# Optimization experiments

Measured on AMD Instinct MI355X. Metric: run time of the kernel, lower is better.

The kernel has to match this reference:

```python
import jax, jax.numpy as jnp
import numpy as np

SCENE = (128, 128, 8)      # (X, Y, Z) voxel grid
VOXEL_SIZE = 0.4
DOWNSAMPLE_Z = 2
NUM_HEADS = 8
NUM_POINTS = 4
LN_EPS = 1e-5


def _pix2vox(depth, K, E, voxel_origin):
    # depth [1,H,W]; K [1,3,3]; E [1,4,4]; voxel_origin [1,3]
    B, H, W = depth.shape
    gx, gy = jnp.meshgrid(jnp.arange(W, dtype=depth.dtype), jnp.arange(H, dtype=depth.dtype))
    pix = jnp.stack([gx, gy])                              # [2,H,W] -> (u, v) after flip in torch
    d = depth[:, None]                                     # [B,1,H,W]
    p_x = jnp.concatenate([pix[None] * d, d], 1).reshape(B, 3, -1)
    p_c = jnp.linalg.inv(K) @ p_x                          # camera coords [B,3,HW]
    p_c = jnp.concatenate([p_c, jnp.ones_like(p_c[:, :1])], 1)
    p_w = jnp.linalg.inv(E) @ p_c                          # world coords [B,4,HW]
    p_v = (jnp.swapaxes(p_w[:, :3], 1, 2) - voxel_origin[:, None, :]) / VOXEL_SIZE - 0.5
    p_v = p_v.at[..., 2].set(p_v[..., 2] / DOWNSAMPLE_Z)
    return jnp.trunc(p_v).astype(jnp.int32)               # torch .long() truncates toward 0


def _voxel_mask(p_v):
    X, Y, Z = SCENE
    p = p_v[0]                                             # [HW,3] (batch asserted == 1)
    valid = ((p[:, 0] >= 0) & (p[:, 0] < X) & (p[:, 1] >= 0) & (p[:, 1] < Y)
             & (p[:, 2] >= 0) & (p[:, 2] < Z))
    flat = jnp.where(valid, (p[:, 0] * Y + p[:, 1]) * Z + p[:, 2], 0)
    return jnp.zeros(X * Y * Z, dtype=bool).at[flat].max(valid)


def _ms_deform_attn(q, feats, ref, Wv, bv, Woff, boff, Wattw, battw, Wout, bout):
    # q [N,C]; feats: list of [C,Hl,Wl]; ref [N,2] normalized (shared across levels)
    N, C = q.shape
    hd = C // NUM_HEADS
    shapes = [(f.shape[1], f.shape[2]) for f in feats]
    L = len(feats)
    flat = jnp.concatenate([f.reshape(C, -1).T for f in feats], 0)      # [Lsum, C]
    value = (flat @ Wv.T + bv).reshape(-1, NUM_HEADS, hd)               # [Lsum, h, hd]
    off = (q @ Woff.T + boff).reshape(N, NUM_HEADS, L, NUM_POINTS, 2)
    w = jax.nn.softmax((q @ Wattw.T + battw).reshape(N, NUM_HEADS, L * NUM_POINTS), -1)
    w = w.reshape(N, NUM_HEADS, L, NUM_POINTS)
    normalizer = jnp.array([[wl, hl] for (hl, wl) in shapes], dtype=q.dtype)  # (W,H) per level
    loc = ref[:, None, None, None, :] + off / normalizer[None, None, :, None, :]
    h_idx = jnp.arange(NUM_HEADS)[None, :, None]
    out = jnp.zeros((N, NUM_HEADS, hd), q.dtype)
    start = 0
    for lvl, (Hl, Wl) in enumerate(shapes):
        v = value[start:start + Hl * Wl]                   # [Hl*Wl, h, hd]
        start += Hl * Wl
        # grid_sample bilinear, align_corners=False, zero padding
        x = loc[:, :, lvl, :, 0] * Wl - 0.5                # [N,h,P]
        y = loc[:, :, lvl, :, 1] * Hl - 0.5
        x0 = jnp.floor(x); y0 = jnp.floor(y)
        lx = x - x0; ly = y - y0
        x0i = x0.astype(jnp.int32); y0i = y0.astype(jnp.int32)
        samp = jnp.zeros((N, NUM_HEADS, NUM_POINTS, hd), q.dtype)
        for dy, dx, wgt in ((0, 0, (1 - lx) * (1 - ly)), (0, 1, lx * (1 - ly)),
                            (1, 0, (1 - lx) * ly), (1, 1, lx * ly)):
            xi = x0i + dx; yi = y0i + dy
            ok = (xi >= 0) & (xi < Wl) & (yi >= 0) & (yi < Hl)
            idx = jnp.where(ok, yi * Wl + xi, 0)
            g = v[idx, h_idx]                              # [N,h,P,hd] per-head gather
            samp = samp + g * (wgt * ok)[..., None]
        out = out + jnp.einsum('nhp,nhpd->nhd', w[:, :, lvl], samp)
    return out.reshape(N, C) @ Wout.T + bout


def _forward(scene_embed, feat0, feat1, feat2, depth, K, E, voxel_origin, ref_pix,
             Wv, bv, Woff, boff, Wattw, battw, Wout, bout, ln_g, ln_b):
    X, Y, Z = SCENE
    mask = _voxel_mask(_pix2vox(depth, K, E, voxel_origin))             # [N] bool
    q = scene_embed[0]                                                  # [N,C]
    attn = _ms_deform_attn(q, [feat0[0], feat1[0], feat2[0]], ref_pix[0],
                           Wv, bv, Woff, boff, Wattw, battw, Wout, bout)
    h = q + attn                                                        # residual (MSDeformAttn identity)
    mu = jnp.mean(h, -1, keepdims=True)
    var = jnp.mean((h - mu) ** 2, -1, keepdims=True)
    h = (h - mu) / jnp.sqrt(var + LN_EPS) * ln_g + ln_b                 # post-norm
    out = jnp.where(mask[:, None], h, q)                                # index_fov_back_to_voxels
    return out.T.reshape(1, -1, X, Y, Z)                                # nlc -> nchw [1,C,X,Y,Z]


def setup_inputs() -> dict:
    key = jax.random.key(0)
    ks = jax.random.split(key, 12)
    X, Y, Z = SCENE
    N = X * Y * Z
    C = 128
    H, W = 192, 640
    s = 0.02
    scene_embed = jax.random.normal(ks[0], (1, N, C), jnp.float32)
    feat0 = jax.random.normal(ks[1], (1, C, 48, 160), jnp.float32)
    feat1 = jax.random.normal(ks[2], (1, C, 24, 80), jnp.float32)
    feat2 = jax.random.normal(ks[3], (1, C, 12, 40), jnp.float32)
    depth = jax.random.uniform(ks[4], (1, H, W), jnp.float32, 1.0, 40.0)
    K = jnp.array([[[552.55, 0.0, 320.0], [0.0, 552.55, 96.0], [0.0, 0.0, 1.0]]], jnp.float32)
    E = jnp.eye(4, dtype=jnp.float32)[None]
    voxel_origin = jnp.array([[-25.6, -3.2, 0.0]], jnp.float32)
    ref_pix = jax.random.uniform(ks[5], (1, N, 2), jnp.float32)
    return {
        'scene_embed': scene_embed, 'feat0': feat0, 'feat1': feat1, 'feat2': feat2,
        'depth': depth, 'K': K, 'E': E, 'voxel_origin': voxel_origin, 'ref_pix': ref_pix,
        'Wv': jax.random.normal(ks[6], (C, C), jnp.float32) * s,
        'bv': jnp.zeros((C,), jnp.float32),
        'Woff': jax.random.normal(ks[7], (NUM_HEADS * 3 * NUM_POINTS * 2, C), jnp.float32) * s,
        'boff': jnp.zeros((NUM_HEADS * 3 * NUM_POINTS * 2,), jnp.float32),
        'Wattw': jax.random.normal(ks[8], (NUM_HEADS * 3 * NUM_POINTS, C), jnp.float32) * s,
        'battw': jnp.zeros((NUM_HEADS * 3 * NUM_POINTS,), jnp.float32),
        'Wout': jax.random.normal(ks[9], (C, C), jnp.float32) * s,
        'bout': jnp.zeros((C,), jnp.float32),
        'ln_g': jnp.ones((C,), jnp.float32),
        'ln_b': jnp.zeros((C,), jnp.float32),
    }


def reference(scene_embed, feat0, feat1, feat2, depth, K, E, voxel_origin, ref_pix,
              Wv, bv, Woff, boff, Wattw, battw, Wout, bout, ln_g, ln_b):
    return _forward(scene_embed, feat0, feat1, feat2, depth, K, E, voxel_origin, ref_pix,
                    Wv, bv, Woff, boff, Wattw, battw, Wout, bout, ln_g, ln_b)
```

## Files before the change

### kernel.cpp

```cpp
#include <hip/hip_runtime.h>
#include <hip/hip_bf16.h>
#include <stdint.h>

#define XS 128
#define YS 128
#define ZS 8
#define NQ (XS*YS*ZS)
#define CDIM 128
#define NH 8
#define HD 16
#define DH 192
#define DW 640
#define NPIX (DH*DW)
#define NVPIX 10080

typedef float f32x4 __attribute__((ext_vector_type(4)));
typedef short s16x8 __attribute__((ext_vector_type(8)));

__device__ __forceinline__ float b2f(unsigned short u){
    union { unsigned int i; float f; } v; v.i = ((unsigned int)u) << 16; return v.f;
}
__device__ __forceinline__ unsigned short f2b(float f){
    __hip_bfloat16 h = __float2bfloat16(f);
    return *reinterpret_cast<unsigned short*>(&h);
}
__device__ __forceinline__ float blo(unsigned int u){
    union { unsigned int i; float f; } v; v.i = u << 16; return v.f;
}
__device__ __forceinline__ float bhi(unsigned int u){
    union { unsigned int i; float f; } v; v.i = u & 0xffff0000u; return v.f;
}

__global__ __launch_bounds__(256)
void inv_kernel(const float* __restrict__ K,
                const float* __restrict__ E,
                double* __restrict__ inv_out,
                const float* __restrict__ Woff,
                const float* __restrict__ Wattw,
                const float* __restrict__ Wout,
                unsigned short* __restrict__ Wbf){
    if (blockIdx.x != 0){
        int idx = (blockIdx.x-1)*256 + threadIdx.x;
        if (idx < 24576)      Wbf[idx] = f2b(Woff[idx]);
        else if (idx < 36864) Wbf[idx] = f2b(Wattw[idx-24576]);
        else if (idx < 40960) Wbf[idx] = 0;
        else if (idx < 57344) Wbf[idx] = f2b(Wout[idx-40960]);
        return;
    }
    if (threadIdx.x != 0) return;
    double k[3][3], e[4][4];
    for (int i=0;i<9;i++)  k[i/3][i%3] = (double)K[i];
    for (int i=0;i<16;i++) e[i/4][i%4] = (double)E[i];
    double det = k[0][0]*(k[1][1]*k[2][2]-k[1][2]*k[2][1])
               - k[0][1]*(k[1][0]*k[2][2]-k[1][2]*k[2][0])
               + k[0][2]*(k[1][0]*k[2][1]-k[1][1]*k[2][0]);
    double id = 1.0/det;
    double inv[3][3];
    inv[0][0]=(k[1][1]*k[2][2]-k[1][2]*k[2][1])*id;
    inv[0][1]=(k[0][2]*k[2][1]-k[0][1]*k[2][2])*id;
    inv[0][2]=(k[0][1]*k[1][2]-k[0][2]*k[1][1])*id;
    inv[1][0]=(k[1][2]*k[2][0]-k[1][0]*k[2][2])*id;
    inv[1][1]=(k[0][0]*k[2][2]-k[0][2]*k[2][0])*id;
    inv[1][2]=(k[0][2]*k[1][0]-k[0][0]*k[1][2])*id;
    inv[2][0]=(k[1][0]*k[2][1]-k[1][1]*k[2][0])*id;
    inv[2][1]=(k[0][1]*k[2][0]-k[0][0]*k[2][1])*id;
    inv[2][2]=(k[0][0]*k[1][1]-k[0][1]*k[1][0])*id;
    for (int i=0;i<9;i++) inv_out[i] = inv[i/3][i%3];
    double a[4][8];
    for (int i=0;i<4;i++){ for(int j=0;j<4;j++){ a[i][j]=e[i][j]; a[i][4+j]=(i==j)?1.0:0.0; } }
    for (int c=0;c<4;c++){
        int piv=c; double best=fabs(a[c][c]);
        for (int r=c+1;r<4;r++){ double v=fabs(a[r][c]); if (v>best){best=v;piv=r;} }
        if (piv!=c){ for (int j=0;j<8;j++){ double tmp=a[c][j]; a[c][j]=a[piv][j]; a[piv][j]=tmp; } }
        double pv = 1.0/a[c][c];
        for (int j=0;j<8;j++) a[c][j]*=pv;
        for (int r=0;r<4;r++){
            if (r==c) continue;
            double f=a[r][c];
            for(int j=0;j<8;j++) a[r][j]-=f*a[c][j];
        }
    }
    for (int i=0;i<16;i++) inv_out[9+i] = a[i/4][4 + (i%4)];
}

__global__ __launch_bounds__(256)
void prep_kernel(const float* __restrict__ q_in,
                 const unsigned short* __restrict__ Wbf,
                 const float* __restrict__ boff,
                 const float* __restrict__ battw,
                 unsigned short* __restrict__ offawB,
                 int nOff, int nVal,
                 const float* __restrict__ f0,
                 const float* __restrict__ f1,
                 const float* __restrict__ f2,
                 const float* __restrict__ Wv,
                 const float* __restrict__ bv,
                 unsigned short* __restrict__ value,
                 const float* __restrict__ depth,
                 const double* __restrict__ invm,
                 const float* __restrict__ vorigin,
                 unsigned char* __restrict__ mask){
    __shared__ __align__(16) unsigned char smem[38016];
    const int t = threadIdx.x;

    if ((int)blockIdx.x < nOff){
        unsigned short* Ob   = (unsigned short*)smem;
        unsigned char*  qbfB = smem;
        float*          bias = (float*)(smem + 36864);
        const int n0 = blockIdx.x * 64;

        #pragma unroll
        for (int i=0;i<8;i++){
            int idx = t + i*256;
            int row = idx >> 5, c4 = idx & 31;
            float4 qv = ((const float4*)(q_in + (size_t)(n0+row)*CDIM))[c4];
            unsigned int pk0 = (unsigned int)f2b(qv.x) | ((unsigned int)f2b(qv.y)<<16);
            unsigned int pk1 = (unsigned int)f2b(qv.z) | ((unsigned int)f2b(qv.w)<<16);
            unsigned int bo = ((unsigned int)(row*256 + c4*8)) ^ (unsigned int)((row&7)<<4);
            *(unsigned int*)(qbfB + bo)     = pk0;
            *(unsigned int*)(qbfB + bo + 4) = pk1;
        }
        for (int i=t;i<288;i+=256) bias[i] = (i<192)? boff[i] : battw[i-192];
        __syncthreads();

        const int w = t >> 6, lane = t & 63, lr = lane & 15, lg = lane >> 4;
        const int nt0 = w*5;
        f32x4 acc[5][4];
        #pragma unroll
        for (int j=0;j<5;j++)
            #pragma unroll
            for (int qt=0;qt<4;qt++) acc[j][qt] = (f32x4){0.f,0.f,0.f,0.f};

        #pragma unroll
        for (int ks=0; ks<4; ++ks){
            s16x8 bf[4];
            #pragma unroll
            for (int qt=0;qt<4;qt++){
                int qrow = qt*16 + lr;
                unsigned int bo = ((unsigned int)(qrow*256 + ks*64 + lg*16)) ^ (unsigned int)((qrow&7)<<4);
                bf[qt] = *(const s16x8*)(qbfB + bo);
            }
            const unsigned short* wp = Wbf + (size_t)(nt0*16 + lr)*CDIM + ks*32 + lg*8;
            #pragma unroll
            for (int j=0;j<5;++j){
                s16x8 af = *(const s16x8*)(wp + j*16*CDIM);
                #pragma unroll
                for (int qt=0;qt<4;qt++)
                    acc[j][qt] = __builtin_amdgcn_mfma_f32_16x16x32_bf16(af, bf[qt], acc[j][qt], 0, 0, 0);
            }
        }
        __syncthreads();

        #pragma unroll
        for (int j=0;j<5;++j){
            int nt = nt0 + j;
            if (nt < 18){
                #pragma unroll
                for (int qt=0;qt<4;qt++){
                    int q = qt*16 + lr;
                    int base = (q>>3)*2304 + (q&7);
                    #pragma unroll
                    for (int r=0;r<4;++r){
                        int f = nt*16 + lg*4 + r;
                        Ob[base + f*8] = f2b(acc[j][qt][r] + bias[f]);
                    }
                }
            }
        }
        __syncthreads();

        for (int task = t; task < 512; task += 256){
            int q = task >> 3, h = task & 7;
            unsigned short* p = Ob + (q>>3)*2304 + (192 + h*12)*8 + (q&7);
            float e[12]; float m = -1e30f;
            #pragma unroll
            for (int i=0;i<12;i++){ e[i] = b2f(p[i*8]); m = fmaxf(m, e[i]); }
            float s = 0.f;
            #pragma unroll
            for (int i=0;i<12;i++){ e[i] = __expf(e[i]-m); s += e[i]; }
            float is = 1.f/s;
            #pragma unroll
            for (int i=0;i<12;i++) p[i*8] = f2b(e[i]*is);
        }
        __syncthreads();

        {
            const uint4* src = (const uint4*)Ob;
            uint4* dst = (uint4*)(offawB + (size_t)blockIdx.x * 18432);
            for (int idx = t; idx < 2304; idx += 256) dst[idx] = src[idx];
        }
    } else if ((int)blockIdx.x < nOff + nVal){
        const int half = t >> 7, tt = t & 127;
        const int p0 = (blockIdx.x - nOff)*8 + half*4;
        float (*fl)[4] = (float(*)[4])(smem + half*2048);
        const float* src; int hw, lp;
        if (p0 < 7680)      { src=f0; hw=7680; lp=p0; }
        else if (p0 < 9600) { src=f1; hw=1920; lp=p0-7680; }
        else                { src=f2; hw=480;  lp=p0-9600; }
        float4 v = *(const float4*)(src + tt*hw + lp);
        fl[tt][0]=v.x; fl[tt][1]=v.y; fl[tt][2]=v.z; fl[tt][3]=v.w;
        __syncthreads();
        float bb = bv[tt];
        float acc[4] = {bb,bb,bb,bb};
        const float4* wrow = (const float4*)(Wv + tt*CDIM);
        #pragma unroll 8
        for (int kc=0; kc<32; ++kc){
            float4 w = wrow[kc];
            #pragma unroll
            for (int u=0;u<4;u++){
                float wu = (u==0)?w.x:(u==1)?w.y:(u==2)?w.z:w.w;
                float4 fv = *(const float4*)fl[kc*4+u];
                acc[0] += fv.x*wu; acc[1] += fv.y*wu; acc[2] += fv.z*wu; acc[3] += fv.w*wu;
            }
        }
        const int hh = tt >> 4, cc = tt & 15;
        #pragma unroll
        for (int i=0;i<4;i++)
            value[((size_t)hh*NVPIX + (size_t)(p0+i))*HD + cc] = f2b(acc[i]);
    } else {
        int tid = (blockIdx.x - nOff - nVal)*256 + t;
        if (tid >= NPIX) return;
        int gx = tid % DW, gy = tid / DW;
        double d  = (double)depth[tid];
        double X0 = (double)gx * d, X1 = (double)gy * d, X2 = d;
        double c0 = invm[0]*X0 + invm[1]*X1 + invm[2]*X2;
        double c1 = invm[3]*X0 + invm[4]*X1 + invm[5]*X2;
        double c2 = invm[6]*X0 + invm[7]*X1 + invm[8]*X2;
        const double* iE = invm + 9;
        double w0 = iE[0]*c0 + iE[1]*c1 + iE[2]*c2  + iE[3];
        double w1 = iE[4]*c0 + iE[5]*c1 + iE[6]*c2  + iE[7];
        double w2 = iE[8]*c0 + iE[9]*c1 + iE[10]*c2 + iE[11];
        double v0 = (w0-(double)vorigin[0])/0.4 - 0.5;
        double v1 = (w1-(double)vorigin[1])/0.4 - 0.5;
        double v2 = ((w2-(double)vorigin[2])/0.4 - 0.5) / 2.0;
        int xi = (int)v0, yi = (int)v1, zi = (int)v2;
        if (xi>=0 && xi<XS && yi>=0 && yi<YS && zi>=0 && zi<ZS)
            mask[(xi*YS + yi)*ZS + zi] = 1;
    }
}

__global__ __launch_bounds__(256, 2)
void attn_kernel(const float* __restrict__ q_in,
                 const float* __restrict__ refpix,
                 const unsigned short* __restrict__ offawB,
                 const unsigned short* __restrict__ value,
                 const unsigned short* __restrict__ WoutBf,
                 const float* __restrict__ bout,
                 const float* __restrict__ lng,
                 const float* __restrict__ lnb,
                 const unsigned char* __restrict__ mask,
                 float* __restrict__ dout,
                 int q0g){
    const int n0l = blockIdx.x * 8;
    const int n0g = q0g + n0l;
    const int t = threadIdx.x;
    __shared__ __align__(16) unsigned char smem[25296];
    unsigned short* raw   = (unsigned short*)(smem);
    unsigned char*  descB = smem + 4608;
    float*          out2  = (float*)(smem + 4608);
    unsigned char*  obfB  = smem + 16896;
    float (*q_s)[CDIM]    = (float(*)[CDIM])(smem + 20992);
    float*          rp_s  = (float*)(smem + 25088);
    float*          wredp = (float*)(smem + 25152);
    unsigned char*  mask_s= (unsigned char*)(smem + 25280);

    {
        const unsigned int* src = (const unsigned int*)(offawB + (size_t)(n0l>>3)*2304);
        unsigned int* dst = (unsigned int*)raw;
        #pragma unroll
        for (int i=0;i<5;i++){ int idx = t + i*256; if (idx < 1152) dst[idx] = src[idx]; }
        ((float4*)q_s)[t] = ((const float4*)(q_in + (size_t)n0g*CDIM))[t];
        ((unsigned int*)obfB)[512 + t] = 0;
        ((unsigned int*)obfB)[768 + t] = 0;
        if (t < 16) rp_s[t] = refpix[n0g*2 + t];
        if (t < 8)  mask_s[t] = mask[n0g + t];
    }
    __syncthreads();

    for (int idx = t; idx < 768; idx += 256){
        int q = idx & 7, hp = idx >> 3;
        int lp = hp % 12;
        float fw, fh; int Wl, Hl, st;
        if (lp < 4)      { fw=160.f; fh=48.f; Wl=160; Hl=48; st=0; }
        else if (lp < 8) { fw=80.f;  fh=24.f; Wl=80;  Hl=24; st=7680; }
        else             { fw=40.f;  fh=12.f; Wl=40;  Hl=12; st=9600; }
        float offx = b2f(raw[(hp*2)*8 + q]);
        float offy = b2f(raw[(hp*2+1)*8 + q]);
        float aw   = b2f(raw[(192+hp)*8 + q]);
        float x = rp_s[q*2+0]*fw - 0.5f + offx;
        float y = rp_s[q*2+1]*fh - 0.5f + offy;
        float x0f = floorf(x), y0f = floorf(y);
        float lx = x-x0f, ly = y-y0f;
        int x0 = (int)x0f, y0 = (int)y0f;
        bool x0ok = (x0>=0)&&(x0<Wl), x1ok=(x0+1>=0)&&(x0+1<Wl);
        bool y0ok = (y0>=0)&&(y0<Hl), y1ok=(y0+1>=0)&&(y0+1<Hl);
        float w00 = (x0ok&&y0ok)? (1.f-lx)*(1.f-ly)*aw : 0.f;
        float w01 = (x1ok&&y0ok)? lx*(1.f-ly)*aw       : 0.f;
        float w10 = (x0ok&&y1ok)? (1.f-lx)*ly*aw       : 0.f;
        float w11 = (x1ok&&y1ok)? lx*ly*aw             : 0.f;
        int yc0 = min(max(y0,0),Hl-1), yc1 = min(max(y0+1,0),Hl-1);
        int xc0 = min(max(x0,0),Wl-1), xc1 = min(max(x0+1,0),Wl-1);
        unsigned int rb0 = (unsigned int)(st + yc0*Wl), rb1 = (unsigned int)(st + yc1*Wl);
        uint4 d;
        d.x = (rb0+(unsigned int)xc0) | ((rb0+(unsigned int)xc1)<<16);
        d.y = (rb1+(unsigned int)xc0) | ((rb1+(unsigned int)xc1)<<16);
        d.z = (unsigned int)f2b(w00) | ((unsigned int)f2b(w01)<<16);
        d.w = (unsigned int)f2b(w10) | ((unsigned int)f2b(w11)<<16);
        *(uint4*)(descB + (((unsigned int)(idx ^ ((idx>>5)&7)))<<4)) = d;
    }
    __syncthreads();

    {
        const int cp = t & 7, hs = (t>>3) & 7, qgs = t >> 6;
        const unsigned int vbase = (unsigned int)hs*(NVPIX*HD*2) + (unsigned int)cp*4;
        const char* vb = (const char*)value;
        float av0x=0.f, av0y=0.f, av1x=0.f, av1y=0.f;
        #pragma unroll
        for (int lp=0; lp<12; ++lp){
            #pragma unroll
            for (int qi2=0; qi2<2; ++qi2){
                int idx = (hs*12+lp)*8 + qgs*2 + qi2;
                uint4 d = *(const uint4*)(descB + (((unsigned int)(idx ^ ((idx>>5)&7)))<<4));
                unsigned int o00 = vbase + ((d.x & 0xffffu)<<5);
                unsigned int o01 = vbase + ((d.x >> 16)<<5);
                unsigned int o10 = vbase + ((d.y & 0xffffu)<<5);
                unsigned int o11 = vbase + ((d.y >> 16)<<5);
                unsigned int u00 = *(const unsigned int*)(vb + o00);
                unsigned int u01 = *(const unsigned int*)(vb + o01);
                unsigned int u10 = *(const unsigned int*)(vb + o10);
                unsigned int u11 = *(const unsigned int*)(vb + o11);
                float w00 = blo(d.z), w01 = bhi(d.z), w10 = blo(d.w), w11 = bhi(d.w);
                float sx = blo(u00)*w00 + blo(u01)*w01 + blo(u10)*w10 + blo(u11)*w11;
                float sy = bhi(u00)*w00 + bhi(u01)*w01 + bhi(u10)*w10 + bhi(u11)*w11;
                if (qi2 == 0){ av0x += sx; av0y += sy; }
                else         { av1x += sx; av1y += sy; }
            }
        }
        const int q0q = qgs*2;
        unsigned int pk0 = (unsigned int)f2b(av0x) | ((unsigned int)f2b(av0y)<<16);
        unsigned int pk1 = (unsigned int)f2b(av1x) | ((unsigned int)f2b(av1y)<<16);
        unsigned int bo0 = (unsigned int)(q0q*256 + hs*32 + cp*4)     ^ (unsigned int)((q0q&7)<<4);
        unsigned int bo1 = (unsigned int)((q0q+1)*256 + hs*32 + cp*4) ^ (unsigned int)(((q0q+1)&7)<<4);
        *(unsigned int*)(obfB + bo0) = pk0;
        *(unsigned int*)(obfB + bo1) = pk1;
    }
    __syncthreads();

    {
        const int w = t >> 6, lane = t & 63, lr = lane & 15, lg = lane >> 4;
        f32x4 a0 = (f32x4){0.f,0.f,0.f,0.f};
        f32x4 a1 = (f32x4){0.f,0.f,0.f,0.f};
        #pragma unroll
        for (int ks=0; ks<4; ++ks){
            unsigned int bo = (unsigned int)(lr*256 + ks*64 + lg*16) ^ (unsigned int)((lr&7)<<4);
            s16x8 bfrag = *(const s16x8*)(obfB + bo);
            const unsigned short* wp = WoutBf + (size_t)(w*32 + lr)*CDIM + ks*32 + lg*8;
            s16x8 af0 = *(const s16x8*)(wp);
            s16x8 af1 = *(const s16x8*)(wp + 16*CDIM);
            a0 = __builtin_amdgcn_mfma_f32_16x16x32_bf16(af0, bfrag, a0, 0, 0, 0);
            a1 = __builtin_amdgcn_mfma_f32_16x16x32_bf16(af1, bfrag, a1, 0, 0, 0);
        }
        if (lr < 8){
            int f0 = w*32 + lg*4;
            float4 b0 = *(const float4*)(bout + f0);
            float4 b1 = *(const float4*)(bout + f0 + 16);
            float4 v0, v1;
            v0.x = a0[0]+b0.x; v0.y = a0[1]+b0.y; v0.z = a0[2]+b0.z; v0.w = a0[3]+b0.w;
            v1.x = a1[0]+b1.x; v1.y = a1[1]+b1.y; v1.z = a1[2]+b1.z; v1.w = a1[3]+b1.w;
            *(float4*)(out2 + lr*CDIM + f0)      = v0;
            *(float4*)(out2 + lr*CDIM + f0 + 16) = v1;
        }
    }
    __syncthreads();

    const int r = t & 127;
    const int qb = t >> 7;
    const int wv = t >> 6;
    float acc[4];
    #pragma unroll
    for (int qi4=0;qi4<4;qi4++) acc[qi4] = out2[(qb*4+qi4)*CDIM + r];

    float hv[4], s1[4], s2[4];
    #pragma unroll
    for (int qi4=0;qi4<4;qi4++){
        hv[qi4] = q_s[qb*4+qi4][r] + acc[qi4];
        s1[qi4] = hv[qi4];
        s2[qi4] = hv[qi4]*hv[qi4];
    }
    #pragma unroll
    for (int off=32; off>0; off>>=1){
        #pragma unroll
        for (int qi4=0;qi4<4;qi4++){
            s1[qi4] += __shfl_xor(s1[qi4], off, 64);
            s2[qi4] += __shfl_xor(s2[qi4], off, 64);
        }
    }
    if ((t&63)==0){
        #pragma unroll
        for (int qi4=0;qi4<4;qi4++){
            wredp[0*16 + wv*4 + qi4] = s1[qi4];
            wredp[1*16 + wv*4 + qi4] = s2[qi4];
        }
    }
    __syncthreads();

    float res[4];
    const float g = lng[r], b = lnb[r];
    #pragma unroll
    for (int qi4=0;qi4<4;qi4++){
        float mu  = (wredp[0*16 + (qb*2)*4 + qi4] + wredp[0*16 + (qb*2+1)*4 + qi4]) * (1.f/128.f);
        float msq = (wredp[1*16 + (qb*2)*4 + qi4] + wredp[1*16 + (qb*2+1)*4 + qi4]) * (1.f/128.f);
        float var = msq - mu*mu;
        float nv  = (hv[qi4]-mu) * __frsqrt_rn(var + 1e-5f) * g + b;
        res[qi4] = mask_s[qb*4+qi4] ? nv : q_s[qb*4+qi4][r];
    }
    float4 o; o.x=res[0]; o.y=res[1]; o.z=res[2]; o.w=res[3];
    *(float4*)(dout + (size_t)r*NQ + n0g + qb*4) = o;
}

extern "C" void kernel_launch(void* const* d_in, const int* in_sizes, int n_in,
                              void* d_out, int out_size, void* d_ws, size_t ws_size,
                              hipStream_t stream){
    const float* scene  = (const float*)d_in[0];
    const float* f0     = (const float*)d_in[1];
    const float* f1     = (const float*)d_in[2];
    const float* f2     = (const float*)d_in[3];
    const float* depth  = (const float*)d_in[4];
    const float* K      = (const float*)d_in[5];
    const float* E      = (const float*)d_in[6];
    const float* vorig  = (const float*)d_in[7];
    const float* refpix = (const float*)d_in[8];
    const float* Wv     = (const float*)d_in[9];
    const float* bv     = (const float*)d_in[10];
    const float* Woff   = (const float*)d_in[11];
    const float* boff   = (const float*)d_in[12];
    const float* Wattw  = (const float*)d_in[13];
    const float* battw  = (const float*)d_in[14];
    const float* Wout   = (const float*)d_in[15];
    const float* bout   = (const float*)d_in[16];
    const float* lng    = (const float*)d_in[17];
    const float* lnb    = (const float*)d_in[18];

    char* ws = (char*)d_ws;
    const size_t FIXED = 512 + 131072 + 2580480 + 114688;
    double*         invm   = (double*)(ws);
    unsigned char*  mask   = (unsigned char*)(ws + 512);
    unsigned short* value  = (unsigned short*)(ws + 512 + 131072);
    unsigned short* Wbf    = (unsigned short*)(ws + 512 + 131072 + 2580480);
    unsigned short* WoutBf = Wbf + 40960;
    unsigned short* offawB = (unsigned short*)(ws + FIXED);

    size_t avail = (ws_size > FIXED) ? (ws_size - FIXED) : 0;
    long long maxq = (long long)(avail / (288*2));
    int chunk = (int)((maxq/64)*64);
    if (chunk > NQ) chunk = NQ;
    if (chunk < 64) chunk = 64;

    hipMemsetAsync(mask, 0, NQ, stream);
    inv_kernel<<<225, 256, 0, stream>>>(K, E, invm, Woff, Wattw, Wout, Wbf);

    for (int q0 = 0; q0 < NQ; q0 += chunk){
        int len = (NQ - q0 < chunk) ? (NQ - q0) : chunk;
        int nOff  = len/64;
        int nVal  = (q0 == 0) ? (NVPIX/8) : 0;
        int nMask = (q0 == 0) ? ((NPIX+255)/256) : 0;
        prep_kernel<<<nOff + nVal + nMask, 256, 0, stream>>>(
            scene + (size_t)q0*CDIM, Wbf, boff, battw, offawB,
            nOff, nVal,
            f0, f1, f2, Wv, bv, value,
            depth, invm, vorig, mask);
        attn_kernel<<<len/8, 256, 0, stream>>>(scene, refpix, offawB, value,
                                               WoutBf, bout, lng, lnb, mask,
                                               (float*)d_out, q0);
    }
}
```

Baseline: 422.5 us.

## Fuse offset/attention-weight projection into attention kernel, drop workspace round trip

```diff
diff --git a/kernel.cpp b/kernel.cpp
--- a/kernel.cpp
+++ b/kernel.cpp
@@ -84,115 +84,23 @@
 }
 
 __global__ __launch_bounds__(256)
-void prep_kernel(const float* __restrict__ q_in,
-                 const unsigned short* __restrict__ Wbf,
-                 const float* __restrict__ boff,
-                 const float* __restrict__ battw,
-                 unsigned short* __restrict__ offawB,
-                 int nOff, int nVal,
-                 const float* __restrict__ f0,
-                 const float* __restrict__ f1,
-                 const float* __restrict__ f2,
-                 const float* __restrict__ Wv,
-                 const float* __restrict__ bv,
-                 unsigned short* __restrict__ value,
-                 const float* __restrict__ depth,
-                 const double* __restrict__ invm,
-                 const float* __restrict__ vorigin,
-                 unsigned char* __restrict__ mask){
-    __shared__ __align__(16) unsigned char smem[38016];
+void prep2_kernel(int nVal,
+                  const float* __restrict__ f0,
+                  const float* __restrict__ f1,
+                  const float* __restrict__ f2,
+                  const float* __restrict__ Wv,
+                  const float* __restrict__ bv,
+                  unsigned short* __restrict__ value,
+                  const float* __restrict__ depth,
+                  const double* __restrict__ invm,
+                  const float* __restrict__ vorigin,
+                  unsigned char* __restrict__ mask){
+    __shared__ float fl2[2][CDIM][4];
     const int t = threadIdx.x;
-
-    if ((int)blockIdx.x < nOff){
-        unsigned short* Ob   = (unsigned short*)smem;
-        unsigned char*  qbfB = smem;
-        float*          bias = (float*)(smem + 36864);
-        const int n0 = blockIdx.x * 64;
-
-        #pragma unroll
-        for (int i=0;i<8;i++){
-            int idx = t + i*256;
-            int row = idx >> 5, c4 = idx & 31;
-            float4 qv = ((const float4*)(q_in + (size_t)(n0+row)*CDIM))[c4];
-            unsigned int pk0 = (unsigned int)f2b(qv.x) | ((unsigned int)f2b(qv.y)<<16);
-            unsigned int pk1 = (unsigned int)f2b(qv.z) | ((unsigned int)f2b(qv.w)<<16);
-            unsigned int bo = ((unsigned int)(row*256 + c4*8)) ^ (unsigned int)((row&7)<<4);
-            *(unsigned int*)(qbfB + bo)     = pk0;
-            *(unsigned int*)(qbfB + bo + 4) = pk1;
-        }
-        for (int i=t;i<288;i+=256) bias[i] = (i<192)? boff[i] : battw[i-192];
-        __syncthreads();
-
-        const int w = t >> 6, lane = t & 63, lr = lane & 15, lg = lane >> 4;
-        const int nt0 = w*5;
-        f32x4 acc[5][4];
-        #pragma unroll
-        for (int j=0;j<5;j++)
-            #pragma unroll
-            for (int qt=0;qt<4;qt++) acc[j][qt] = (f32x4){0.f,0.f,0.f,0.f};
-
-        #pragma unroll
-        for (int ks=0; ks<4; ++ks){
-            s16x8 bf[4];
-            #pragma unroll
-            for (int qt=0;qt<4;qt++){
-                int qrow = qt*16 + lr;
-                unsigned int bo = ((unsigned int)(qrow*256 + ks*64 + lg*16)) ^ (unsigned int)((qrow&7)<<4);
-                bf[qt] = *(const s16x8*)(qbfB + bo);
-            }
-            const unsigned short* wp = Wbf + (size_t)(nt0*16 + lr)*CDIM + ks*32 + lg*8;
-            #pragma unroll
-            for (int j=0;j<5;++j){
-                s16x8 af = *(const s16x8*)(wp + j*16*CDIM);
-                #pragma unroll
-                for (int qt=0;qt<4;qt++)
-                    acc[j][qt] = __builtin_amdgcn_mfma_f32_16x16x32_bf16(af, bf[qt], acc[j][qt], 0, 0, 0);
-            }
-        }
-        __syncthreads();
-
-        #pragma unroll
-        for (int j=0;j<5;++j){
-            int nt = nt0 + j;
-            if (nt < 18){
-                #pragma unroll
-                for (int qt=0;qt<4;qt++){
-                    int q = qt*16 + lr;
-                    int base = (q>>3)*2304 + (q&7);
-                    #pragma unroll
-                    for (int r=0;r<4;++r){
-                        int f = nt*16 + lg*4 + r;
-                        Ob[base + f*8] = f2b(acc[j][qt][r] + bias[f]);
-                    }
-                }
-            }
-        }
-        __syncthreads();
-
-        for (int task = t; task < 512; task += 256){
-            int q = task >> 3, h = task & 7;
-            unsigned short* p = Ob + (q>>3)*2304 + (192 + h*12)*8 + (q&7);
-            float e[12]; float m = -1e30f;
-            #pragma unroll
-            for (int i=0;i<12;i++){ e[i] = b2f(p[i*8]); m = fmaxf(m, e[i]); }
-            float s = 0.f;
-            #pragma unroll
-            for (int i=0;i<12;i++){ e[i] = __expf(e[i]-m); s += e[i]; }
-            float is = 1.f/s;
-            #pragma unroll
-            for (int i=0;i<12;i++) p[i*8] = f2b(e[i]*is);
-        }
-        __syncthreads();
-
-        {
-            const uint4* src = (const uint4*)Ob;
-            uint4* dst = (uint4*)(offawB + (size_t)blockIdx.x * 18432);
-            for (int idx = t; idx < 2304; idx += 256) dst[idx] = src[idx];
-        }
-    } else if ((int)blockIdx.x < nOff + nVal){
+    if ((int)blockIdx.x < nVal){
         const int half = t >> 7, tt = t & 127;
-        const int p0 = (blockIdx.x - nOff)*8 + half*4;
-        float (*fl)[4] = (float(*)[4])(smem + half*2048);
+        const int p0 = blockIdx.x*8 + half*4;
+        float (*fl)[4] = fl2[half];
         const float* src; int hw, lp;
         if (p0 < 7680)      { src=f0; hw=7680; lp=p0; }
         else if (p0 < 9600) { src=f1; hw=1920; lp=p0-7680; }
@@ -218,7 +126,7 @@
         for (int i=0;i<4;i++)
             value[((size_t)hh*NVPIX + (size_t)(p0+i))*HD + cc] = f2b(acc[i]);
     } else {
-        int tid = (blockIdx.x - nOff - nVal)*256 + t;
+        int tid = (blockIdx.x - nVal)*256 + t;
         if (tid >= NPIX) return;
         int gx = tid % DW, gy = tid / DW;
         double d  = (double)depth[tid];
@@ -240,182 +148,250 @@
 }
 
 __global__ __launch_bounds__(256, 2)
-void attn_kernel(const float* __restrict__ q_in,
-                 const float* __restrict__ refpix,
-                 const unsigned short* __restrict__ offawB,
-                 const unsigned short* __restrict__ value,
-                 const unsigned short* __restrict__ WoutBf,
-                 const float* __restrict__ bout,
-                 const float* __restrict__ lng,
-                 const float* __restrict__ lnb,
-                 const unsigned char* __restrict__ mask,
-                 float* __restrict__ dout,
-                 int q0g){
-    const int n0l = blockIdx.x * 8;
-    const int n0g = q0g + n0l;
+void attn_fused(const float* __restrict__ q_in,
+                const float* __restrict__ refpix,
+                const unsigned short* __restrict__ Wbf,
+                const float* __restrict__ boff,
+                const float* __restrict__ battw,
+                const unsigned short* __restrict__ value,
+                const unsigned short* __restrict__ WoutBf,
+                const float* __restrict__ bout,
+                const float* __restrict__ lng,
+                const float* __restrict__ lnb,
+                const unsigned char* __restrict__ mask,
+                float* __restrict__ dout){
+    const int nq0 = blockIdx.x * 32;
     const int t = threadIdx.x;
-    __shared__ __align__(16) unsigned char smem[25296];
-    unsigned short* raw   = (unsigned short*)(smem);
-    unsigned char*  descB = smem + 4608;
-    float*          out2  = (float*)(smem + 4608);
-    unsigned char*  obfB  = smem + 16896;
-    float (*q_s)[CDIM]    = (float(*)[CDIM])(smem + 20992);
-    float*          rp_s  = (float*)(smem + 25088);
-    float*          wredp = (float*)(smem + 25152);
-    unsigned char*  mask_s= (unsigned char*)(smem + 25280);
-
-    {
-        const unsigned int* src = (const unsigned int*)(offawB + (size_t)(n0l>>3)*2304);
-        unsigned int* dst = (unsigned int*)raw;
-        #pragma unroll
-        for (int i=0;i<5;i++){ int idx = t + i*256; if (idx < 1152) dst[idx] = src[idx]; }
-        ((float4*)q_s)[t] = ((const float4*)(q_in + (size_t)n0g*CDIM))[t];
-        ((unsigned int*)obfB)[512 + t] = 0;
-        ((unsigned int*)obfB)[768 + t] = 0;
-        if (t < 16) rp_s[t] = refpix[n0g*2 + t];
-        if (t < 8)  mask_s[t] = mask[n0g + t];
-    }
-    __syncthreads();
-
-    for (int idx = t; idx < 768; idx += 256){
-        int q = idx & 7, hp = idx >> 3;
-        int lp = hp % 12;
-        float fw, fh; int Wl, Hl, st;
-        if (lp < 4)      { fw=160.f; fh=48.f; Wl=160; Hl=48; st=0; }
-        else if (lp < 8) { fw=80.f;  fh=24.f; Wl=80;  Hl=24; st=7680; }
-        else             { fw=40.f;  fh=12.f; Wl=40;  Hl=12; st=9600; }
-        float offx = b2f(raw[(hp*2)*8 + q]);
-        float offy = b2f(raw[(hp*2+1)*8 + q]);
-        float aw   = b2f(raw[(192+hp)*8 + q]);
-        float x = rp_s[q*2+0]*fw - 0.5f + offx;
-        float y = rp_s[q*2+1]*fh - 0.5f + offy;
-        float x0f = floorf(x), y0f = floorf(y);
-        float lx = x-x0f, ly = y-y0f;
-        int x0 = (int)x0f, y0 = (int)y0f;
-        bool x0ok = (x0>=0)&&(x0<Wl), x1ok=(x0+1>=0)&&(x0+1<Wl);
-        bool y0ok = (y0>=0)&&(y0<Hl), y1ok=(y0+1>=0)&&(y0+1<Hl);
-        float w00 = (x0ok&&y0ok)? (1.f-lx)*(1.f-ly)*aw : 0.f;
-        float w01 = (x1ok&&y0ok)? lx*(1.f-ly)*aw       : 0.f;
-        float w10 = (x0ok&&y1ok)? (1.f-lx)*ly*aw       : 0.f;
-        float w11 = (x1ok&&y1ok)? lx*ly*aw             : 0.f;
-        int yc0 = min(max(y0,0),Hl-1), yc1 = min(max(y0+1,0),Hl-1);
-        int xc0 = min(max(x0,0),Wl-1), xc1 = min(max(x0+1,0),Wl-1);
-        unsigned int rb0 = (unsigned int)(st + yc0*Wl), rb1 = (unsigned int)(st + yc1*Wl);
-        uint4 d;
-        d.x = (rb0+(unsigned int)xc0) | ((rb0+(unsigned int)xc1)<<16);
-        d.y = (rb1+(unsigned int)xc0) | ((rb1+(unsigned int)xc1)<<16);
-        d.z = (unsigned int)f2b(w00) | ((unsigned int)f2b(w01)<<16);
-        d.w = (unsigned int)f2b(w10) | ((unsigned int)f2b(w11)<<16);
-        *(uint4*)(descB + (((unsigned int)(idx ^ ((idx>>5)&7)))<<4)) = d;
-    }
-    __syncthreads();
-
-    {
-        const int cp = t & 7, hs = (t>>3) & 7, qgs = t >> 6;
-        const unsigned int vbase = (unsigned int)hs*(NVPIX*HD*2) + (unsigned int)cp*4;
-        const char* vb = (const char*)value;
-        float av0x=0.f, av0y=0.f, av1x=0.f, av1y=0.f;
-        #pragma unroll
-        for (int lp=0; lp<12; ++lp){
-            #pragma unroll
-            for (int qi2=0; qi2<2; ++qi2){
-                int idx = (hs*12+lp)*8 + qgs*2 + qi2;
-                uint4 d = *(const uint4*)(descB + (((unsigned int)(idx ^ ((idx>>5)&7)))<<4));
-                unsigned int o00 = vbase + ((d.x & 0xffffu)<<5);
-                unsigned int o01 = vbase + ((d.x >> 16)<<5);
-                unsigned int o10 = vbase + ((d.y & 0xffffu)<<5);
-                unsigned int o11 = vbase + ((d.y >> 16)<<5);
-                unsigned int u00 = *(const unsigned int*)(vb + o00);
-                unsigned int u01 = *(const unsigned int*)(vb + o01);
-                unsigned int u10 = *(const unsigned int*)(vb + o10);
-                unsigned int u11 = *(const unsigned int*)(vb + o11);
-                float w00 = blo(d.z), w01 = bhi(d.z), w10 = blo(d.w), w11 = bhi(d.w);
-                float sx = blo(u00)*w00 + blo(u01)*w01 + blo(u10)*w10 + blo(u11)*w11;
-                float sy = bhi(u00)*w00 + bhi(u01)*w01 + bhi(u10)*w10 + bhi(u11)*w11;
-                if (qi2 == 0){ av0x += sx; av0y += sy; }
-                else         { av1x += sx; av1y += sy; }
-            }
-        }
-        const int q0q = qgs*2;
-        unsigned int pk0 = (unsigned int)f2b(av0x) | ((unsigned int)f2b(av0y)<<16);
-        unsigned int pk1 = (unsigned int)f2b(av1x) | ((unsigned int)f2b(av1y)<<16);
-        unsigned int bo0 = (unsigned int)(q0q*256 + hs*32 + cp*4)     ^ (unsigned int)((q0q&7)<<4);
-        unsigned int bo1 = (unsigned int)((q0q+1)*256 + hs*32 + cp*4) ^ (unsigned int)(((q0q+1)&7)<<4);
-        *(unsigned int*)(obfB + bo0) = pk0;
-        *(unsigned int*)(obfB + bo1) = pk1;
-    }
+    __shared__ __align__(16) unsigned char smem[36384];
+    unsigned short* Ob    = (unsigned short*)smem;
+    unsigned char*  qbfB  = smem + 18432;
+    unsigned char*  descB = smem + 18432;
+    float*          out2  = (float*)(smem + 18432);
+    unsigned char*  obfB  = smem + 30720;
+    float*          bias  = (float*)(smem + 34816);
+    float*          rp_s  = (float*)(smem + 35968);
+    unsigned char*  mask_s= smem + 36224;
+    float*          wredp = (float*)(smem + 36256);
+
+    #pragma unroll
+    for (int i=0;i<4;i++){
+        int idx = t + i*256;
+        int row = idx >> 5, c4 = idx & 31;
+        float4 qv = ((const float4*)(q_in + (size_t)(nq0+row)*CDIM))[c4];
+        unsigned int pk0 = (unsigned int)f2b(qv.x) | ((unsigned int)f2b(qv.y)<<16);
+        unsigned int pk1 = (unsigned int)f2b(qv.z) | ((unsigned int)f2b(qv.w)<<16);
+        unsigned int bo = ((unsigned int)(row*256 + c4*8)) ^ (unsigned int)((row&7)<<4);
+        *(unsigned int*)(qbfB + bo)     = pk0;
+        *(unsigned int*)(qbfB + bo + 4) = pk1;
+    }
+    for (int i=t;i<288;i+=256) bias[i] = (i<192)? boff[i] : battw[i-192];
+    ((unsigned int*)obfB)[512 + t] = 0;
+    ((unsigned int*)obfB)[768 + t] = 0;
+    if (t < 64) rp_s[t] = refpix[nq0*2 + t];
+    if (t < 32) mask_s[t] = mask[nq0 + t];
     __syncthreads();
 
     {
         const int w = t >> 6, lane = t & 63, lr = lane & 15, lg = lane >> 4;
-        f32x4 a0 = (f32x4){0.f,0.f,0.f,0.f};
-        f32x4 a1 = (f32x4){0.f,0.f,0.f,0.f};
+        const int nt0 = w*5;
+        f32x4 acc[5][2];
+        #pragma unroll
+        for (int j=0;j<5;j++){ acc[j][0]=(f32x4){0,0,0,0}; acc[j][1]=(f32x4){0,0,0,0}; }
         #pragma unroll
         for (int ks=0; ks<4; ++ks){
-            unsigned int bo = (unsigned int)(lr*256 + ks*64 + lg*16) ^ (unsigned int)((lr&7)<<4);
-            s16x8 bfrag = *(const s16x8*)(obfB + bo);
-            const unsigned short* wp = WoutBf + (size_t)(w*32 + lr)*CDIM + ks*32 + lg*8;
-            s16x8 af0 = *(const s16x8*)(wp);
-            s16x8 af1 = *(const s16x8*)(wp + 16*CDIM);
-            a0 = __builtin_amdgcn_mfma_f32_16x16x32_bf16(af0, bfrag, a0, 0, 0, 0);
-            a1 = __builtin_amdgcn_mfma_f32_16x16x32_bf16(af1, bfrag, a1, 0, 0, 0);
-        }
-        if (lr < 8){
-            int f0 = w*32 + lg*4;
-            float4 b0 = *(const float4*)(bout + f0);
-            float4 b1 = *(const float4*)(bout + f0 + 16);
-            float4 v0, v1;
-            v0.x = a0[0]+b0.x; v0.y = a0[1]+b0.y; v0.z = a0[2]+b0.z; v0.w = a0[3]+b0.w;
-            v1.x = a1[0]+b1.x; v1.y = a1[1]+b1.y; v1.z = a1[2]+b1.z; v1.w = a1[3]+b1.w;
-            *(float4*)(out2 + lr*CDIM + f0)      = v0;
-            *(float4*)(out2 + lr*CDIM + f0 + 16) = v1;
+            s16x8 bf[2];
+            #pragma unroll
+            for (int qt=0;qt<2;qt++){
+                int qrow = qt*16 + lr;
+                unsigned int bo = ((unsigned int)(qrow*256 + ks*64 + lg*16)) ^ (unsigned int)((qrow&7)<<4);
+                bf[qt] = *(const s16x8*)(qbfB + bo);
+            }
+            const unsigned short* wp = Wbf + (size_t)(nt0*16 + lr)*CDIM + ks*32 + lg*8;
+            #pragma unroll
+            for (int j=0;j<5;++j){
+                s16x8 af = *(const s16x8*)(wp + j*16*CDIM);
+                acc[j][0] = __builtin_amdgcn_mfma_f32_16x16x32_bf16(af, bf[0], acc[j][0], 0, 0, 0);
+                acc[j][1] = __builtin_amdgcn_mfma_f32_16x16x32_bf16(af, bf[1], acc[j][1], 0, 0, 0);
+            }
+        }
+        #pragma unroll
+        for (int j=0;j<5;++j){
+            int nt = nt0 + j;
+            if (nt < 18){
+                #pragma unroll
+                for (int qt=0;qt<2;qt++){
+                    int q = qt*16 + lr;
+                    int base = (q>>3)*2304 + (q&7);
+                    #pragma unroll
+                    for (int r=0;r<4;++r){
+                        int f = nt*16 + lg*4 + r;
+                        Ob[base + f*8] = f2b(acc[j][qt][r] + bias[f]);
+                    }
+                }
+            }
         }
     }
     __syncthreads();
 
-    const int r = t & 127;
-    const int qb = t >> 7;
-    const int wv = t >> 6;
-    float acc[4];
-    #pragma unroll
-    for (int qi4=0;qi4<4;qi4++) acc[qi4] = out2[(qb*4+qi4)*CDIM + r];
-
-    float hv[4], s1[4], s2[4];
-    #pragma unroll
-    for (int qi4=0;qi4<4;qi4++){
-        hv[qi4] = q_s[qb*4+qi4][r] + acc[qi4];
-        s1[qi4] = hv[qi4];
-        s2[qi4] = hv[qi4]*hv[qi4];
-    }
-    #pragma unroll
-    for (int off=32; off>0; off>>=1){
-        #pragma unroll
-        for (int qi4=0;qi4<4;qi4++){
-            s1[qi4] += __shfl_xor(s1[qi4], off, 64);
-            s2[qi4] += __shfl_xor(s2[qi4], off, 64);
-        }
-    }
-    if ((t&63)==0){
-        #pragma unroll
-        for (int qi4=0;qi4<4;qi4++){
-            wredp[0*16 + wv*4 + qi4] = s1[qi4];
-            wredp[1*16 + wv*4 + qi4] = s2[qi4];
-        }
+    {
+        int q = t >> 3, h = t & 7;
+        unsigned short* p = Ob + (q>>3)*2304 + (192 + h*12)*8 + (q&7);
+        float e[12]; float m = -1e30f;
+        #pragma unroll
+        for (int i=0;i<12;i++){ e[i] = b2f(p[i*8]); m = fmaxf(m, e[i]); }
+        float s = 0.f;
+        #pragma unroll
+        for (int i=0;i<12;i++){ e[i] = __expf(e[i]-m); s += e[i]; }
+        float is = 1.f/s;
+        #pragma unroll
+        for (int i=0;i<12;i++) p[i*8] = f2b(e[i]*is);
     }
     __syncthreads();
 
-    float res[4];
-    const float g = lng[r], b = lnb[r];
-    #pragma unroll
-    for (int qi4=0;qi4<4;qi4++){
-        float mu  = (wredp[0*16 + (qb*2)*4 + qi4] + wredp[0*16 + (qb*2+1)*4 + qi4]) * (1.f/128.f);
-        float msq = (wredp[1*16 + (qb*2)*4 + qi4] + wredp[1*16 + (qb*2+1)*4 + qi4]) * (1.f/128.f);
-        float var = msq - mu*mu;
-        float nv  = (hv[qi4]-mu) * __frsqrt_rn(var + 1e-5f) * g + b;
-        res[qi4] = mask_s[qb*4+qi4] ? nv : q_s[qb*4+qi4][r];
-    }
-    float4 o; o.x=res[0]; o.y=res[1]; o.z=res[2]; o.w=res[3];
-    *(float4*)(dout + (size_t)r*NQ + n0g + qb*4) = o;
+    for (int sr = 0; sr < 4; ++sr){
+        const unsigned short* raw = Ob + sr*2304;
+        const int nsr = nq0 + sr*8;
+
+        for (int idx = t; idx < 768; idx += 256){
+            int q = idx & 7, hp = idx >> 3;
+            int lp = hp % 12;
+            float fw, fh; int Wl, Hl, st;
+            if (lp < 4)      { fw=160.f; fh=48.f; Wl=160; Hl=48; st=0; }
+            else if (lp < 8) { fw=80.f;  fh=24.f; Wl=80;  Hl=24; st=7680; }
+            else             { fw=40.f;  fh=12.f; Wl=40;  Hl=12; st=9600; }
+            float offx = b2f(raw[(hp*2)*8 + q]);
+            float offy = b2f(raw[(hp*2+1)*8 + q]);
+            float aw   = b2f(raw[(192+hp)*8 + q]);
+            float x = rp_s[(sr*8+q)*2+0]*fw - 0.5f + offx;
+            float y = rp_s[(sr*8+q)*2+1]*fh - 0.5f + offy;
+            float x0f = floorf(x), y0f = floorf(y);
+            float lx = x-x0f, ly = y-y0f;
+            int x0 = (int)x0f, y0 = (int)y0f;
+            bool x0ok = (x0>=0)&&(x0<Wl), x1ok=(x0+1>=0)&&(x0+1<Wl);
+            bool y0ok = (y0>=0)&&(y0<Hl), y1ok=(y0+1>=0)&&(y0+1<Hl);
+            float w00 = (x0ok&&y0ok)? (1.f-lx)*(1.f-ly)*aw : 0.f;
+            float w01 = (x1ok&&y0ok)? lx*(1.f-ly)*aw       : 0.f;
+            float w10 = (x0ok&&y1ok)? (1.f-lx)*ly*aw       : 0.f;
+            float w11 = (x1ok&&y1ok)? lx*ly*aw             : 0.f;
+            int yc0 = min(max(y0,0),Hl-1), yc1 = min(max(y0+1,0),Hl-1);
+            int xc0 = min(max(x0,0),Wl-1), xc1 = min(max(x0+1,0),Wl-1);
+            unsigned int rb0 = (unsigned int)(st + yc0*Wl), rb1 = (unsigned int)(st + yc1*Wl);
+            uint4 d;
+            d.x = (rb0+(unsigned int)xc0) | ((rb0+(unsigned int)xc1)<<16);
+            d.y = (rb1+(unsigned int)xc0) | ((rb1+(unsigned int)xc1)<<16);
+            d.z = (unsigned int)f2b(w00) | ((unsigned int)f2b(w01)<<16);
+            d.w = (unsigned int)f2b(w10) | ((unsigned int)f2b(w11)<<16);
+            *(uint4*)(descB + (((unsigned int)(idx ^ ((idx>>5)&7)))<<4)) = d;
+        }
+        __syncthreads();
+
+        {
+            const int cp = t & 7, hs = (t>>3) & 7, qgs = t >> 6;
+            const unsigned int vbase = (unsigned int)hs*(NVPIX*HD*2) + (unsigned int)cp*4;
+            const char* vb = (const char*)value;
+            float av0x=0.f, av0y=0.f, av1x=0.f, av1y=0.f;
+            #pragma unroll
+            for (int lp=0; lp<12; ++lp){
+                #pragma unroll
+                for (int qi2=0; qi2<2; ++qi2){
+                    int idx = (hs*12+lp)*8 + qgs*2 + qi2;
+                    uint4 d = *(const uint4*)(descB + (((unsigned int)(idx ^ ((idx>>5)&7)))<<4));
+                    unsigned int o00 = vbase + ((d.x & 0xffffu)<<5);
+                    unsigned int o01 = vbase + ((d.x >> 16)<<5);
+                    unsigned int o10 = vbase + ((d.y & 0xffffu)<<5);
+                    unsigned int o11 = vbase + ((d.y >> 16)<<5);
+                    unsigned int u00 = *(const unsigned int*)(vb + o00);
+                    unsigned int u01 = *(const unsigned int*)(vb + o01);
+                    unsigned int u10 = *(const unsigned int*)(vb + o10);
+                    unsigned int u11 = *(const unsigned int*)(vb + o11);
+                    float w00 = blo(d.z), w01 = bhi(d.z), w10 = blo(d.w), w11 = bhi(d.w);
+                    float sx = blo(u00)*w00 + blo(u01)*w01 + blo(u10)*w10 + blo(u11)*w11;
+                    float sy = bhi(u00)*w00 + bhi(u01)*w01 + bhi(u10)*w10 + bhi(u11)*w11;
+                    if (qi2 == 0){ av0x += sx; av0y += sy; }
+                    else         { av1x += sx; av1y += sy; }
+                }
+            }
+            const int q0q = qgs*2;
+            unsigned int pk0 = (unsigned int)f2b(av0x) | ((unsigned int)f2b(av0y)<<16);
+            unsigned int pk1 = (unsigned int)f2b(av1x) | ((unsigned int)f2b(av1y)<<16);
+            unsigned int bo0 = (unsigned int)(q0q*256 + hs*32 + cp*4)     ^ (unsigned int)((q0q&7)<<4);
+            unsigned int bo1 = (unsigned int)((q0q+1)*256 + hs*32 + cp*4) ^ (unsigned int)(((q0q+1)&7)<<4);
+            *(unsigned int*)(obfB + bo0) = pk0;
+            *(unsigned int*)(obfB + bo1) = pk1;
+        }
+        __syncthreads();
+
+        {
+            const int w = t >> 6, lane = t & 63, lr = lane & 15, lg = lane >> 4;
+            f32x4 a0 = (f32x4){0.f,0.f,0.f,0.f};
+            f32x4 a1 = (f32x4){0.f,0.f,0.f,0.f};
+            #pragma unroll
+            for (int ks=0; ks<4; ++ks){
+                unsigned int bo = (unsigned int)(lr*256 + ks*64 + lg*16) ^ (unsigned int)((lr&7)<<4);
+                s16x8 bfrag = *(const s16x8*)(obfB + bo);
+                const unsigned short* wp = WoutBf + (size_t)(w*32 + lr)*CDIM + ks*32 + lg*8;
+                s16x8 af0 = *(const s16x8*)(wp);
+                s16x8 af1 = *(const s16x8*)(wp + 16*CDIM);
+                a0 = __builtin_amdgcn_mfma_f32_16x16x32_bf16(af0, bfrag, a0, 0, 0, 0);
+                a1 = __builtin_amdgcn_mfma_f32_16x16x32_bf16(af1, bfrag, a1, 0, 0, 0);
+            }
+            if (lr < 8){
+                int f0 = w*32 + lg*4;
+                float4 b0 = *(const float4*)(bout + f0);
+                float4 b1 = *(const float4*)(bout + f0 + 16);
+                float4 v0, v1;
+                v0.x = a0[0]+b0.x; v0.y = a0[1]+b0.y; v0.z = a0[2]+b0.z; v0.w = a0[3]+b0.w;
+                v1.x = a1[0]+b1.x; v1.y = a1[1]+b1.y; v1.z = a1[2]+b1.z; v1.w = a1[3]+b1.w;
+                *(float4*)(out2 + lr*CDIM + f0)      = v0;
+                *(float4*)(out2 + lr*CDIM + f0 + 16) = v1;
+            }
+        }
+        __syncthreads();
+
+        {
+            const int r = t & 127;
+            const int qb = t >> 7;
+            const int wv = t >> 6;
+            float qv[4], hv[4], s1[4], s2[4];
+            #pragma unroll
+            for (int qi4=0;qi4<4;qi4++){
+                qv[qi4] = q_in[(size_t)(nsr + qb*4 + qi4)*CDIM + r];
+                hv[qi4] = qv[qi4] + out2[(qb*4+qi4)*CDIM + r];
+                s1[qi4] = hv[qi4];
+                s2[qi4] = hv[qi4]*hv[qi4];
+            }
+            #pragma unroll
+            for (int off=32; off>0; off>>=1){
+                #pragma unroll
+                for (int qi4=0;qi4<4;qi4++){
+                    s1[qi4] += __shfl_xor(s1[qi4], off, 64);
+                    s2[qi4] += __shfl_xor(s2[qi4], off, 64);
+                }
+            }
+            if ((t&63)==0){
+                #pragma unroll
+                for (int qi4=0;qi4<4;qi4++){
+                    wredp[0*16 + wv*4 + qi4] = s1[qi4];
+                    wredp[1*16 + wv*4 + qi4] = s2[qi4];
+                }
+            }
+            __syncthreads();
+
+            float res[4];
+            const float g = lng[r], b = lnb[r];
+            #pragma unroll
+            for (int qi4=0;qi4<4;qi4++){
+                float mu  = (wredp[0*16 + (qb*2)*4 + qi4] + wredp[0*16 + (qb*2+1)*4 + qi4]) * (1.f/128.f);
+                float msq = (wredp[1*16 + (qb*2)*4 + qi4] + wredp[1*16 + (qb*2+1)*4 + qi4]) * (1.f/128.f);
+                float var = msq - mu*mu;
+                float nv  = (hv[qi4]-mu) * __frsqrt_rn(var + 1e-5f) * g + b;
+                res[qi4] = mask_s[sr*8 + qb*4+qi4] ? nv : qv[qi4];
+            }
+            float4 o; o.x=res[0]; o.y=res[1]; o.z=res[2]; o.w=res[3];
+            *(float4*)(dout + (size_t)r*NQ + nsr + qb*4) = o;
+        }
+        __syncthreads();
+    }
 }
 
 extern "C" void kernel_launch(void* const* d_in, const int* in_sizes, int n_in,
@@ -442,35 +418,20 @@
     const float* lnb    = (const float*)d_in[18];
 
     char* ws = (char*)d_ws;
-    const size_t FIXED = 512 + 131072 + 2580480 + 114688;
     double*         invm   = (double*)(ws);
     unsigned char*  mask   = (unsigned char*)(ws + 512);
     unsigned short* value  = (unsigned short*)(ws + 512 + 131072);
     unsigned short* Wbf    = (unsigned short*)(ws + 512 + 131072 + 2580480);
     unsigned short* WoutBf = Wbf + 40960;
-    unsigned short* offawB = (unsigned short*)(ws + FIXED);
-
-    size_t avail = (ws_size > FIXED) ? (ws_size - FIXED) : 0;
-    long long maxq = (long long)(avail / (288*2));
-    int chunk = (int)((maxq/64)*64);
-    if (chunk > NQ) chunk = NQ;
-    if (chunk < 64) chunk = 64;
 
     hipMemsetAsync(mask, 0, NQ, stream);
     inv_kernel<<<225, 256, 0, stream>>>(K, E, invm, Woff, Wattw, Wout, Wbf);
 
-    for (int q0 = 0; q0 < NQ; q0 += chunk){
-        int len = (NQ - q0 < chunk) ? (NQ - q0) : chunk;
-        int nOff  = len/64;
-        int nVal  = (q0 == 0) ? (NVPIX/8) : 0;
-        int nMask = (q0 == 0) ? ((NPIX+255)/256) : 0;
-        prep_kernel<<<nOff + nVal + nMask, 256, 0, stream>>>(
-            scene + (size_t)q0*CDIM, Wbf, boff, battw, offawB,
-            nOff, nVal,
-            f0, f1, f2, Wv, bv, value,
-            depth, invm, vorig, mask);
-        attn_kernel<<<len/8, 256, 0, stream>>>(scene, refpix, offawB, value,
-                                               WoutBf, bout, lng, lnb, mask,
-                                               (float*)d_out, q0);
-    }
-}
+    int nVal  = NVPIX/8;
+    int nMask = (NPIX+255)/256;
+    prep2_kernel<<<nVal + nMask, 256, 0, stream>>>(nVal, f0, f1, f2, Wv, bv, value,
+                                                   depth, invm, vorig, mask);
+    attn_fused<<<NQ/32, 256, 0, stream>>>(scene, refpix, Wbf, boff, battw, value,
+                                          WoutBf, bout, lng, lnb, mask,
+                                          (float*)d_out);
+}
```

Measured after the change: 401.8 us. -4.9%, faster.
